# Kernel tuning notes

Hardware: AMD Instinct MI355X
Metric: run time of the kernel (lower is better)

The kernel has to match this reference:

```python
import jax, jax.numpy as jnp
import numpy as np

B, T, C = 2, 4096, 2048
HS = 64
H = C // HS            # 32 heads
D_W, D_A, D_MV, D_G = 128, 128, 64, 224
EPS_GN = 0.00064
EPS_NORM = 1e-12


def setup_inputs() -> dict:
    key = jax.random.key(0)
    ks = jax.random.split(key, 24)
    n = lambda k, s, sc=1.0: (jax.random.normal(k, s, dtype=jnp.float32) * sc)
    inp = {
        "x": n(ks[0], (B, T, C)),
        "v_first": n(ks[1], (B, T, C)),
        "y": n(ks[2], (B, T, C)),
        # token-shift mixing coefficients [1,1,C]
        "x_r": n(ks[3], (1, 1, C), 0.1), "x_w": n(ks[4], (1, 1, C), 0.1),
        "x_k": n(ks[5], (1, 1, C), 0.1), "x_v": n(ks[6], (1, 1, C), 0.1),
        "x_a": n(ks[7], (1, 1, C), 0.1), "x_g": n(ks[8], (1, 1, C), 0.1),
        # decay LoRA
        "w0": n(ks[9], (1, 1, C), 0.5) - 3.0,
        "w1": n(ks[10], (C, D_W), 0.02), "w2": n(ks[11], (D_W, C), 0.02),
        # in-context-rate LoRA
        "a0": n(ks[12], (1, 1, C), 0.2),
        "a1": n(ks[13], (C, D_A), 0.02), "a2": n(ks[14], (D_A, C), 0.02),
        # value-mix LoRA
        "v0": n(ks[15], (1, 1, C), 0.2) + 0.73,
        "v1": n(ks[16], (C, D_MV), 0.02), "v2": n(ks[17], (D_MV, C), 0.02),
        # gate LoRA
        "g1": n(ks[18], (C, D_G), 0.02), "g2": n(ks[19], (D_G, C), 0.02),
        "k_k": jnp.full((1, 1, C), 0.71, dtype=jnp.float32),
        "k_a": jnp.full((1, 1, C), 1.02, dtype=jnp.float32),
        "r_k": jnp.full((H, HS), -0.04, dtype=jnp.float32),
        # square projections
        "W_r": n(ks[20], (C, C), 0.5 / C ** 0.5),
        "W_k": n(ks[21], (C, C), 0.05 / C ** 0.5),
        "W_v": n(ks[22], (C, C), 0.5 / C ** 0.5),
        "W_o": n(ks[23], (C, C), 0.02),
        "ln_g": jnp.ones((C,), dtype=jnp.float32),
        "ln_b": jnp.zeros((C,), dtype=jnp.float32),
    }
    return inp


def reference(x, v_first, y, x_r, x_w, x_k, x_v, x_a, x_g,
              w0, w1, w2, a0, a1, a2, v0, v1, v2, g1, g2,
              k_k, k_a, r_k, W_r, W_k, W_v, W_o, ln_g, ln_b):
    Bx, Tx, Cx = x.shape
    Hn, hs = r_k.shape

    # ---- project ----
    xx = jnp.pad(x[:, :-1, :], ((0, 0), (1, 0), (0, 0))) - x  # time_shift_1(x) - x
    xr = x + xx * x_r
    xw = x + xx * x_w
    xk = x + xx * x_k
    xv = x + xx * x_v
    xa = x + xx * x_a
    xg = x + xx * x_g

    r = xr @ W_r.T
    w = -jax.nn.softplus(-(w0 + jnp.tanh(xw @ w1) @ w2)) - 0.5
    k = xk @ W_k.T
    v = xv @ W_v.T
    # layer_id == 1 (> 0): mix with v_first
    v = v + (v_first - v) * jax.nn.sigmoid(v0 + (xv @ v1) @ v2)
    a = jax.nn.sigmoid(a0 + (xa @ a1) @ a2)
    g = jax.nn.sigmoid(xg @ g1) @ g2

    kk = k * k_k
    kkh = kk.reshape(Bx, Tx, Hn, hs)
    nrm = jnp.sqrt(jnp.sum(kkh * kkh, axis=-1, keepdims=True))
    kk = (kkh / jnp.maximum(nrm, EPS_NORM)).reshape(Bx, Tx, Cx)
    k = k * (1.0 + (a - 1.0) * k_a)

    # ---- post_kernel ----
    yh = y.reshape(Bx, Tx, Hn, hs)
    mu = jnp.mean(yh, axis=-1, keepdims=True)
    var = jnp.mean((yh - mu) ** 2, axis=-1, keepdims=True)
    yn = ((yh - mu) / jnp.sqrt(var + EPS_GN)).reshape(Bx, Tx, Cx)
    yn = yn * ln_g + ln_b

    rh = r.reshape(Bx, Tx, Hn, hs)
    kh = k.reshape(Bx, Tx, Hn, hs)
    vh = v.reshape(Bx, Tx, Hn, hs)
    dot = jnp.sum(rh * kh * r_k, axis=-1, keepdims=True)  # [B,T,H,1]
    y2 = yn + (dot * vh).reshape(Bx, Tx, Cx)
    out = (y2 * g) @ W_o.T
    return out, w, a, kk
```

## Files before the change

### kernel.cpp

```cpp
#include <hip/hip_runtime.h>
#include <math.h>

typedef unsigned short u16;
typedef __attribute__((ext_vector_type(8))) short short8;
typedef __attribute__((ext_vector_type(4))) float floatx4;
typedef __attribute__((ext_vector_type(4))) unsigned short ushort4v;
typedef __attribute__((ext_vector_type(8))) unsigned short ushort8v;

#define DEV static __device__ __forceinline__

DEV u16 f2b(float f) {
  unsigned u = __builtin_bit_cast(unsigned, f);
  u += 0x7fffu + ((u >> 16) & 1u);
  return (u16)(u >> 16);
}
DEV float b2f(u16 h) { return __builtin_bit_cast(float, ((unsigned)h) << 16); }

DEV void gld16(const u16* g, u16* l) {
  __builtin_amdgcn_global_load_lds((__attribute__((address_space(1))) void*)(g),
                                   (__attribute__((address_space(3))) void*)(l), 16, 0, 0);
}

__global__ __launch_bounds__(256) void ew_mix(
    const float* __restrict__ x,
    const float* __restrict__ cr, const float* __restrict__ ck,
    const float* __restrict__ cv, const float* __restrict__ cw,
    const float* __restrict__ ca, const float* __restrict__ cg,
    u16* __restrict__ oxr, u16* __restrict__ oxk, u16* __restrict__ oxv,
    u16* __restrict__ oxw, u16* __restrict__ oxa, u16* __restrict__ oxg)
{
  const long idx = (long)blockIdx.x * 256 + threadIdx.x;
  const long row = idx >> 8;
  const int c8 = (int)(idx & 255) << 3;
  const long off = (row << 11) + c8;
  const floatx4 xa_ = *(const floatx4*)(x + off);
  const floatx4 xb_ = *(const floatx4*)(x + off + 4);
  floatx4 pa = (floatx4)0.f, pb = (floatx4)0.f;
  if ((row & 4095) != 0) {
    pa = *(const floatx4*)(x + off - 2048);
    pb = *(const floatx4*)(x + off - 2044);
  }
  floatx4 da, db;
#pragma unroll
  for (int i = 0; i < 4; ++i) { da[i] = pa[i] - xa_[i]; db[i] = pb[i] - xb_[i]; }
#define EMIT(cp, op) {                                                         \
    const floatx4 c0 = *(const floatx4*)(cp + c8);                             \
    const floatx4 c1 = *(const floatx4*)(cp + c8 + 4);                         \
    ushort8v o;                                                                \
    _Pragma("unroll")                                                          \
    for (int i = 0; i < 4; ++i) {                                              \
      o[i]     = f2b(xa_[i] + da[i] * c0[i]);                                  \
      o[4 + i] = f2b(xb_[i] + db[i] * c1[i]);                                  \
    }                                                                          \
    *(ushort8v*)(op + off) = o; }
  EMIT(cr, oxr); EMIT(ck, oxk); EMIT(cv, oxv);
  EMIT(cw, oxw); EMIT(ca, oxa); EMIT(cg, oxg);
#undef EMIT
}

__global__ __launch_bounds__(256) void transpose_cast(
    const float* __restrict__ w1, const float* __restrict__ a1,
    const float* __restrict__ v1, const float* __restrict__ g1,
    const float* __restrict__ w2, const float* __restrict__ a2,
    const float* __restrict__ v2, const float* __restrict__ g2,
    u16* __restrict__ w1T, u16* __restrict__ a1T, u16* __restrict__ v1T,
    u16* __restrict__ g1T, u16* __restrict__ w2T, u16* __restrict__ a2T,
    u16* __restrict__ v2T, u16* __restrict__ g2T,
    const float* __restrict__ Wr, const float* __restrict__ Wk,
    const float* __restrict__ Wv, const float* __restrict__ Wo,
    u16* __restrict__ Wr16, u16* __restrict__ Wk16,
    u16* __restrict__ Wv16, u16* __restrict__ Wo16)
{
  const long idx = (long)blockIdx.x * 256 + threadIdx.x;
  if (blockIdx.y >= 8) {
    const float* s; u16* d;
    switch (blockIdx.y) {
      case 8:  s = Wr; d = Wr16; break;
      case 9:  s = Wk; d = Wk16; break;
      case 10: s = Wv; d = Wv16; break;
      default: s = Wo; d = Wo16; break;
    }
    const long i = idx * 8;
    const float4 a = *(const float4*)(s + i);
    const float4 b = *(const float4*)(s + i + 4);
    ushort4v lo = { f2b(a.x), f2b(a.y), f2b(a.z), f2b(a.w) };
    ushort4v hi = { f2b(b.x), f2b(b.y), f2b(b.z), f2b(b.w) };
    *(ushort4v*)(d + i) = lo;
    *(ushort4v*)(d + i + 4) = hi;
    return;
  }
  const float* src; u16* dst; int sk, sn, dn, dk;
  switch (blockIdx.y) {
    case 0: src = w1; dst = w1T; sk = 2048; sn = 128; dn = 128;  dk = 2048; break;
    case 1: src = a1; dst = a1T; sk = 2048; sn = 128; dn = 128;  dk = 2048; break;
    case 2: src = v1; dst = v1T; sk = 2048; sn = 64;  dn = 128;  dk = 2048; break;
    case 3: src = g1; dst = g1T; sk = 2048; sn = 224; dn = 256;  dk = 2048; break;
    case 4: src = w2; dst = w2T; sk = 128;  sn = 2048; dn = 2048; dk = 128; break;
    case 5: src = a2; dst = a2T; sk = 128;  sn = 2048; dn = 2048; dk = 128; break;
    case 6: src = v2; dst = v2T; sk = 64;   sn = 2048; dn = 2048; dk = 128; break;
    default:src = g2; dst = g2T; sk = 224;  sn = 2048; dn = 2048; dk = 256; break;
  }
  const long total = (long)dn * dk;
  if (idx >= total) return;
  const int n = (int)(idx / dk), k = (int)(idx % dk);
  float v = 0.f;
  if (k < sk && n < sn) v = src[(long)k * sn + n];
  dst[idx] = f2b(v);
}

#define GEMM128_BODY(Abase, Bbase, K)                                          \
  floatx4 acc[4][4];                                                           \
  _Pragma("unroll")                                                            \
  for (int i = 0; i < 4; ++i)                                                  \
    _Pragma("unroll")                                                          \
    for (int jq = 0; jq < 4; ++jq) acc[i][jq] = (floatx4)0.f;                  \
  const int nK = (K) >> 6;                                                     \
  for (int kt = 0; kt < nK; ++kt) {                                            \
    const int k0 = kt << 6;                                                    \
    __syncthreads();                                                           \
    _Pragma("unroll")                                                          \
    for (int i = 0; i < 4; ++i) {                                              \
      const int c = i * 256 + tid;                                             \
      const int row = c >> 3;                                                  \
      const int sch = (c & 7) ^ (row & 7);                                     \
      const long goff = (long)row * (K) + k0 + sch * 8;                        \
      const int lbase = (i * 256 + wave * 64) * 8;                             \
      gld16((Abase) + goff, &sA[lbase]);                                       \
      gld16((Bbase) + goff, &sB[lbase]);                                       \
    }                                                                          \
    asm volatile("s_waitcnt vmcnt(0)" ::: "memory");                           \
    __syncthreads();                                                           \
    _Pragma("unroll")                                                          \
    for (int ks = 0; ks < 2; ++ks) {                                           \
      short8 af[4], bfr[4];                                                    \
      _Pragma("unroll")                                                        \
      for (int mi = 0; mi < 4; ++mi) {                                         \
        const int row = wm * 64 + mi * 16 + lrow;                              \
        const int ch = (ks * 4 + lkg) ^ (row & 7);                             \
        af[mi] = *(const short8*)&sA[row * 64 + ch * 8];                       \
      }                                                                        \
      _Pragma("unroll")                                                        \
      for (int ni = 0; ni < 4; ++ni) {                                         \
        const int row = wn * 64 + ni * 16 + lrow;                              \
        const int ch = (ks * 4 + lkg) ^ (row & 7);                             \
        bfr[ni] = *(const short8*)&sB[row * 64 + ch * 8];                      \
      }                                                                        \
      _Pragma("unroll")                                                        \
      for (int mi = 0; mi < 4; ++mi)                                           \
        _Pragma("unroll")                                                      \
        for (int ni = 0; ni < 4; ++ni)                                         \
          acc[mi][ni] = __builtin_amdgcn_mfma_f32_16x16x32_bf16(af[mi], bfr[ni], acc[mi][ni], 0, 0, 0); \
    }                                                                          \
  }

__global__ __launch_bounds__(256, 2) void gemm_s1(
    const u16* __restrict__ xw, const u16* __restrict__ w1T, u16* __restrict__ hw,
    const u16* __restrict__ xa, const u16* __restrict__ a1T, u16* __restrict__ ha,
    const u16* __restrict__ xv, const u16* __restrict__ v1T, u16* __restrict__ hv,
    const u16* __restrict__ xg, const u16* __restrict__ g1T, u16* __restrict__ hg)
{
  __shared__ __align__(16) u16 sA[128 * 64];
  __shared__ __align__(16) u16 sB[128 * 64];
  const int bid = blockIdx.x;
  const int jid = (bid < 64) ? 0 : (bid < 128) ? 1 : (bid < 192) ? 2 : 3;
  const u16* A = (jid == 0) ? xw : (jid == 1) ? xa : (jid == 2) ? xv : xg;
  const u16* B = (jid == 0) ? w1T : (jid == 1) ? a1T : (jid == 2) ? v1T : g1T;
  u16* Cv = (jid == 0) ? hw : (jid == 1) ? ha : (jid == 2) ? hv : hg;
  const int N = (jid == 3) ? 256 : 128;
  const int lb = bid - ((jid == 0) ? 0 : (jid == 1) ? 64 : (jid == 2) ? 128 : 192);
  const int tid = threadIdx.x;
  const int wave = tid >> 6, lane = tid & 63;
  const int lrow = lane & 15, lkg = lane >> 4;
  const int wm = wave >> 1, wn = wave & 1;
  const int nbn = N >> 7;
  const int bm = lb / nbn, bn = lb % nbn;
  const u16* Abase = A + (long)bm * 128 * 2048;
  const u16* Bbase = B + (long)bn * 128 * 2048;

  GEMM128_BODY(Abase, Bbase, 2048)

  const int row0 = bm * 128 + wm * 64 + lkg * 4;
  const int col0 = bn * 128 + wn * 64 + lrow;
#pragma unroll
  for (int mi = 0; mi < 4; ++mi)
#pragma unroll
    for (int ni = 0; ni < 4; ++ni) {
      const int col = col0 + ni * 16;
#pragma unroll
      for (int r = 0; r < 4; ++r) {
        const long o = (long)(row0 + mi * 16 + r) * N + col;
        float v = acc[mi][ni][r];
        if (jid == 0) v = tanhf(v);
        else if (jid == 3) v = 1.f / (1.f + expf(-v));
        Cv[o] = f2b(v);
      }
    }
}

__global__ __launch_bounds__(256, 2) void gemm_s2(
    const u16* __restrict__ hw, const u16* __restrict__ w2T, float* __restrict__ wsec, const float* __restrict__ w0,
    const u16* __restrict__ ha, const u16* __restrict__ a2T, float* __restrict__ asec, const float* __restrict__ a0,
    const u16* __restrict__ hv, const u16* __restrict__ v2T, u16* __restrict__ vs, const float* __restrict__ v0,
    const u16* __restrict__ hg, const u16* __restrict__ g2T, u16* __restrict__ gb)
{
  __shared__ __align__(16) u16 sA[128 * 64];
  __shared__ __align__(16) u16 sB[128 * 64];
  const int jid = blockIdx.x >> 10;
  const int lb = blockIdx.x & 1023;
  const u16* A = (jid == 0) ? hw : (jid == 1) ? ha : (jid == 2) ? hv : hg;
  const u16* B = (jid == 0) ? w2T : (jid == 1) ? a2T : (jid == 2) ? v2T : g2T;
  const float* bias = (jid == 0) ? w0 : (jid == 1) ? a0 : v0;
  const int K = (jid == 3) ? 256 : 128;
  const int tid = threadIdx.x;
  const int wave = tid >> 6, lane = tid & 63;
  const int lrow = lane & 15, lkg = lane >> 4;
  const int wm = wave >> 1, wn = wave & 1;
  const int bm = lb >> 4, bn = lb & 15;
  const u16* Abase = A + (long)bm * 128 * K;
  const u16* Bbase = B + (long)bn * 128 * K;

  GEMM128_BODY(Abase, Bbase, K)

  const int row0 = bm * 128 + wm * 64 + lkg * 4;
  const int col0 = bn * 128 + wn * 64 + lrow;
#pragma unroll
  for (int mi = 0; mi < 4; ++mi)
#pragma unroll
    for (int ni = 0; ni < 4; ++ni) {
      const int col = col0 + ni * 16;
#pragma unroll
      for (int r = 0; r < 4; ++r) {
        const long o = (long)(row0 + mi * 16 + r) * 2048 + col;
        const float v = acc[mi][ni][r];
        if (jid == 0) {
          const float zz = -(v + bias[col]);
          const float sp = fmaxf(zz, 0.f) + log1pf(expf(-fabsf(zz)));
          wsec[o] = -sp - 0.5f;
        } else if (jid == 1) {
          asec[o] = 1.f / (1.f + expf(-(v + bias[col])));
        } else if (jid == 2) {
          vs[o] = f2b(1.f / (1.f + expf(-(v + bias[col]))));
        } else {
          gb[o] = f2b(v);
        }
      }
    }
}

template<int OP>
__global__ __launch_bounds__(512, 2) void gemm256(
    const u16* __restrict__ A0, const u16* __restrict__ B0, void* __restrict__ C0,
    const u16* __restrict__ A1, const u16* __restrict__ B1, void* __restrict__ C1,
    const u16* __restrict__ A2, const u16* __restrict__ B2, void* __restrict__ C2)
{
  __shared__ __align__(16) u16 lds[8 * 8192];
  const int tid = threadIdx.x;
  const int wave = tid >> 6, lane = tid & 63;
  const int lrow = lane & 15, lq = lane >> 4;
  const int wm = wave >> 2, wn = wave & 3;
  const int job = blockIdx.x >> 8;
  const int d = blockIdx.x & 255;
  const int lb = ((d & 7) << 5) | (d >> 3);
  const int bm = lb >> 3, bn = lb & 7;

  const u16* Aj = (job == 0) ? A0 : ((job == 1) ? A1 : A2);
  const u16* Bj = (job == 0) ? B0 : ((job == 1) ? B1 : B2);
  void* Cj      = (job == 0) ? C0 : ((job == 1) ? C1 : C2);

  const u16* __restrict__ Ab = Aj + (long)bm * 256 * 2048;
  const u16* __restrict__ Bb = Bj + (long)bn * 256 * 2048;

  int srco[2], dsto[2];
#pragma unroll
  for (int l = 0; l < 2; ++l) {
    const int c = l * 512 + tid;
    const int row = c >> 2, q = c & 3;
    const int qs = q ^ ((row >> 1) & 3);
    srco[l] = row * 2048 + qs * 8;
    dsto[l] = (l * 512 + wave * 64) * 8;
  }
  int offA[2][4], offB[4];
#pragma unroll
  for (int qm = 0; qm < 2; ++qm)
#pragma unroll
    for (int mi = 0; mi < 4; ++mi) {
      const int r = wm * 128 + qm * 64 + mi * 16 + lrow;
      offA[qm][mi] = r * 32 + (lq ^ ((r >> 1) & 3)) * 8;
    }
#pragma unroll
  for (int ni = 0; ni < 4; ++ni) {
    const int r = wn * 64 + ni * 16 + lrow;
    offB[ni] = r * 32 + (lq ^ ((r >> 1) & 3)) * 8;
  }

  floatx4 acc[8][4];
#pragma unroll
  for (int i = 0; i < 8; ++i)
#pragma unroll
    for (int jq = 0; jq < 4; ++jq) acc[i][jq] = (floatx4)0.f;

#define STAGE(sU, slot) {                                                  \
    const int t_ = (sU) >> 2, j_ = (sU) & 3;                               \
    const u16* base_ = (j_ & 1) ? Bb : Ab;                                 \
    const int kofs_ = t_ * 64 + ((j_ & 2) ? 32 : 0);                       \
    gld16(base_ + srco[0] + kofs_, &lds[(slot) * 8192 + dsto[0]]);         \
    gld16(base_ + srco[1] + kofs_, &lds[(slot) * 8192 + dsto[1]]);         \
  }

#pragma unroll
  for (int s = 0; s < 6; ++s) STAGE(s, s);
  asm volatile("s_waitcnt vmcnt(4)" ::: "memory");
  asm volatile("s_barrier" ::: "memory");

#define SEC(P, sA_, sB_, sS0, sS1)                                             \
  {                                                                            \
    short8 af0[4], af1[4], bfv[4];                                             \
    _Pragma("unroll")                                                          \
    for (int mi = 0; mi < 4; ++mi)                                             \
      af0[mi] = *(const short8*)&lds[(sA_) * 8192 + offA[0][mi]];              \
    _Pragma("unroll")                                                          \
    for (int ni = 0; ni < 4; ++ni)                                             \
      bfv[ni] = *(const short8*)&lds[(sB_) * 8192 + offB[ni]];                 \
    _Pragma("unroll")                                                          \
    for (int mi = 0; mi < 4; ++mi)                                             \
      af1[mi] = *(const short8*)&lds[(sA_) * 8192 + offA[1][mi]];              \
    if ((P) < 61) { asm volatile("s_waitcnt vmcnt(4)" ::: "memory"); }         \
    else          { asm volatile("s_waitcnt vmcnt(0)" ::: "memory"); }         \
    asm volatile("s_barrier" ::: "memory");                                    \
    if ((P) <= 60) {                                                           \
      STAGE(2 * (P) + 6, sS0);                                                 \
      STAGE(2 * (P) + 7, sS1);                                                 \
    }                                                                          \
    _Pragma("unroll")                                                          \
    for (int mi = 0; mi < 4; ++mi)                                             \
      _Pragma("unroll")                                                        \
      for (int ni = 0; ni < 4; ++ni)                                           \
        acc[mi][ni] = __builtin_amdgcn_mfma_f32_16x16x32_bf16(af0[mi], bfv[ni], acc[mi][ni], 0, 0, 0); \
    _Pragma("unroll")                                                          \
    for (int mi = 0; mi < 4; ++mi)                                             \
      _Pragma("unroll")                                                        \
      for (int ni = 0; ni < 4; ++ni)                                           \
        acc[4 + mi][ni] = __builtin_amdgcn_mfma_f32_16x16x32_bf16(af1[mi], bfv[ni], acc[4 + mi][ni], 0, 0, 0); \
  }

  for (int pp = 0; pp < 64; pp += 4) {
    SEC(pp,     0, 1, 6, 7);
    SEC(pp + 1, 2, 3, 0, 1);
    SEC(pp + 2, 4, 5, 2, 3);
    SEC(pp + 3, 6, 7, 4, 5);
  }
#undef SEC
#undef STAGE

  const long row0 = (long)bm * 256 + wm * 128 + lq * 4;
  const int col0 = bn * 256 + wn * 64 + lrow;
#pragma unroll
  for (int mi = 0; mi < 8; ++mi) {
#pragma unroll
    for (int ni = 0; ni < 4; ++ni) {
      const int col = col0 + ni * 16;
#pragma unroll
      for (int r = 0; r < 4; ++r) {
        const long o = (row0 + mi * 16 + r) * 2048 + col;
        const float v = acc[mi][ni][r];
        if constexpr (OP == 0) ((float*)Cj)[o] = v;
        else ((u16*)Cj)[o] = f2b(v);
      }
    }
  }
}

DEV float wsum16(float v) {
  v += __shfl_xor(v, 1);  v += __shfl_xor(v, 2);
  v += __shfl_xor(v, 4);  v += __shfl_xor(v, 8);
  return v;
}

__global__ __launch_bounds__(256) void ew_head(
    const u16* __restrict__ r16, const u16* __restrict__ k16,
    float* __restrict__ kkout,
    const float* __restrict__ abuf,
    const u16* __restrict__ v0buf, const u16* __restrict__ vsbuf,
    const u16* __restrict__ gbuf,
    const float* __restrict__ y, const float* __restrict__ vfirst,
    const float* __restrict__ kkc, const float* __restrict__ kac,
    const float* __restrict__ rk, const float* __restrict__ lng,
    const float* __restrict__ lnb, u16* __restrict__ z)
{
  const int tid = threadIdx.x;
  const long gh = (long)blockIdx.x * 16 + (tid >> 4);
  const long m = gh >> 5;
  const int h = (int)(gh & 31);
  const int li = tid & 15;
  const int c = h * 64 + li * 4;
  const long off = (m << 11) + c;

  const ushort4v k0p = *(const ushort4v*)(k16 + off);
  const floatx4 av   = *(const floatx4*)(abuf + off);
  const floatx4 kkcv = *(const floatx4*)(kkc + c);
  const floatx4 kacv = *(const floatx4*)(kac + c);
  float k0[4], kf[4], kr[4];
  float ss = 0.f;
#pragma unroll
  for (int i = 0; i < 4; ++i) {
    k0[i] = b2f(k0p[i]);
    kf[i] = k0[i] * (1.f + (av[i] - 1.f) * kacv[i]);
    kr[i] = k0[i] * kkcv[i];
    ss += kr[i] * kr[i];
  }
  const float nrm = sqrtf(wsum16(ss));
  const float rn = 1.f / fmaxf(nrm, 1e-12f);
  floatx4 kkv;
#pragma unroll
  for (int i = 0; i < 4; ++i) kkv[i] = kr[i] * rn;
  *(floatx4*)(kkout + off) = kkv;

  const floatx4 yv = *(const floatx4*)(y + off);
  const float mu = wsum16(yv[0] + yv[1] + yv[2] + yv[3]) * 0.015625f;
  float dy[4], sv2 = 0.f;
#pragma unroll
  for (int i = 0; i < 4; ++i) { dy[i] = yv[i] - mu; sv2 += dy[i] * dy[i]; }
  const float var = wsum16(sv2) * 0.015625f;
  const float rs = rsqrtf(var + 0.00064f);
  const floatx4 lngv = *(const floatx4*)(lng + c);
  const floatx4 lnbv = *(const floatx4*)(lnb + c);
  float yn[4];
#pragma unroll
  for (int i = 0; i < 4; ++i) yn[i] = dy[i] * rs * lngv[i] + lnbv[i];

  const ushort4v rp = *(const ushort4v*)(r16 + off);
  const floatx4 rkv = *(const floatx4*)(rk + c);
  float dd = 0.f;
#pragma unroll
  for (int i = 0; i < 4; ++i) dd += b2f(rp[i]) * kf[i] * rkv[i];
  const float dot = wsum16(dd);

  const ushort4v v0p = *(const ushort4v*)(v0buf + off);
  const ushort4v vsp = *(const ushort4v*)(vsbuf + off);
  const floatx4 vfv  = *(const floatx4*)(vfirst + off);
  const ushort4v gp  = *(const ushort4v*)(gbuf + off);
  ushort4v zo;
#pragma unroll
  for (int i = 0; i < 4; ++i) {
    const float v0v = b2f(v0p[i]);
    const float vv = v0v + (vfv[i] - v0v) * b2f(vsp[i]);
    zo[i] = f2b((yn[i] + dot * vv) * b2f(gp[i]));
  }
  *(ushort4v*)(z + off) = zo;
}

extern "C" void kernel_launch(void* const* d_in, const int* in_sizes, int n_in,
                              void* d_out, int out_size, void* d_ws, size_t ws_size,
                              hipStream_t stream)
{
  (void)in_sizes; (void)out_size;
  if (n_in < 29) return;
  const int Mrows = 8192;
  const long C = 2048;
  const long MB_ = (long)Mrows * C;

  const float* x   = (const float*)d_in[0];
  const float* vf  = (const float*)d_in[1];
  const float* y   = (const float*)d_in[2];
  const float* x_r = (const float*)d_in[3];
  const float* x_w = (const float*)d_in[4];
  const float* x_k = (const float*)d_in[5];
  const float* x_v = (const float*)d_in[6];
  const float* x_a = (const float*)d_in[7];
  const float* x_g = (const float*)d_in[8];
  const float* w0  = (const float*)d_in[9];
  const float* w1  = (const float*)d_in[10];
  const float* w2  = (const float*)d_in[11];
  const float* a0  = (const float*)d_in[12];
  const float* a1  = (const float*)d_in[13];
  const float* a2  = (const float*)d_in[14];
  const float* v0  = (const float*)d_in[15];
  const float* v1  = (const float*)d_in[16];
  const float* v2  = (const float*)d_in[17];
  const float* g1  = (const float*)d_in[18];
  const float* g2  = (const float*)d_in[19];
  const float* k_k = (const float*)d_in[20];
  const float* k_a = (const float*)d_in[21];
  const float* r_k = (const float*)d_in[22];
  const float* W_r = (const float*)d_in[23];
  const float* W_k = (const float*)d_in[24];
  const float* W_v = (const float*)d_in[25];
  const float* W_o = (const float*)d_in[26];
  const float* lng = (const float*)d_in[27];
  const float* lnb = (const float*)d_in[28];

  float* out_sec = (float*)d_out;
  float* w_sec   = out_sec + MB_;
  float* a_sec   = w_sec + MB_;
  float* kk_sec  = a_sec + MB_;

  u16* k16 = (u16*)out_sec;
  u16* r16 = (u16*)out_sec + MB_;
  u16* Wr16 = (u16*)w_sec;
  u16* Wk16 = Wr16 + C * C;
  u16* Wv16 = Wk16 + C * C;

  u16* p = (u16*)d_ws;
  u16* xr = p;            p += MB_;
  u16* xk = p;            p += MB_;
  u16* xv = p;            p += MB_;
  u16* xw = p;            p += MB_;
  u16* xa = p;            p += MB_;
  u16* xg = p;            p += MB_;
  u16* Wo16 = p;          p += C * C;
  u16* w1T = p;           p += 128 * C;
  u16* a1T = p;           p += 128 * C;
  u16* v1T = p;           p += 128 * C;
  u16* g1T = p;           p += 256 * C;
  u16* w2T = p;           p += C * 128;
  u16* a2T = p;           p += C * 128;
  u16* v2T = p;           p += C * 128;
  u16* g2T = p;           p += C * 256;
  u16* hw  = p;           p += (long)Mrows * 128;
  u16* ha  = p;           p += (long)Mrows * 128;
  u16* hv  = p;           p += (long)Mrows * 128;
  u16* hg  = p;           p += (long)Mrows * 256;
  const size_t need = (size_t)((char*)p - (char*)d_ws);
  if (ws_size < need) return;

  u16* v0buf = xg;
  u16* zbuf  = xk;
  u16* vsbuf = xw;
  u16* gbuf  = xa;

  ew_mix<<<8192, 256, 0, stream>>>(x, x_r, x_k, x_v, x_w, x_a, x_g,
                                   xr, xk, xv, xw, xa, xg);
  transpose_cast<<<dim3(2048, 12), 256, 0, stream>>>(
      w1, a1, v1, g1, w2, a2, v2, g2,
      w1T, a1T, v1T, g1T, w2T, a2T, v2T, g2T,
      W_r, W_k, W_v, W_o, Wr16, Wk16, Wv16, Wo16);
  gemm_s1<<<320, 256, 0, stream>>>(xw, w1T, hw, xa, a1T, ha,
                                   xv, v1T, hv, xg, g1T, hg);
  gemm256<1><<<768, 512, 0, stream>>>(xr, Wr16, r16,
                                      xk, Wk16, k16,
                                      xv, Wv16, v0buf);
  gemm_s2<<<4096, 256, 0, stream>>>(hw, w2T, w_sec, w0,
                                    ha, a2T, a_sec, a0,
                                    hv, v2T, vsbuf, v0,
                                    hg, g2T, gbuf);
  ew_head<<<16384, 256, 0, stream>>>(r16, k16, kk_sec, a_sec, v0buf, vsbuf, gbuf,
                                     y, vf, k_k, k_a, r_k, lng, lnb, zbuf);
  gemm256<0><<<256, 512, 0, stream>>>(zbuf, Wo16, out_sec,
                                      zbuf, Wo16, out_sec,
                                      zbuf, Wo16, out_sec);
}
```

Measured before the change: 670.5 us.

## Use 4-wave 256x256 GEMM blocks with 128x128 warp tiles and register double-buffered fragments

The 256x256 bf16 GEMM moves from 8 waves (128x64 per wave) to 4 waves (128x128 per wave), which raises MFMA work per LDS fragment load. It also double-buffers the A and B fragments in registers, so fragments for the next K-step are read from LDS while the current MFMAs issue. Each thread now issues 4 global-to-LDS loads per stage, and the wait counts are adjusted to match. The cost is a much larger register footprint (64 accumulators plus 32 fragment registers) and occupancy of one 256-thread block per CU, which risks spills or leaving little latency hiding.

```diff
diff --git a/kernel.cpp b/kernel.cpp
--- a/kernel.cpp
+++ b/kernel.cpp
@@ -248,7 +248,7 @@
 }
 
 template<int OP>
-__global__ __launch_bounds__(512, 2) void gemm256(
+__global__ __launch_bounds__(256, 1) void gemm256(
     const u16* __restrict__ A0, const u16* __restrict__ B0, void* __restrict__ C0,
     const u16* __restrict__ A1, const u16* __restrict__ B1, void* __restrict__ C1,
     const u16* __restrict__ A2, const u16* __restrict__ B2, void* __restrict__ C2)
@@ -257,7 +257,7 @@
   const int tid = threadIdx.x;
   const int wave = tid >> 6, lane = tid & 63;
   const int lrow = lane & 15, lq = lane >> 4;
-  const int wm = wave >> 2, wn = wave & 3;
+  const int wm = wave >> 1, wn = wave & 1;
   const int job = blockIdx.x >> 8;
   const int d = blockIdx.x & 255;
   const int lb = ((d & 7) << 5) | (d >> 3);
@@ -270,62 +270,55 @@
   const u16* __restrict__ Ab = Aj + (long)bm * 256 * 2048;
   const u16* __restrict__ Bb = Bj + (long)bn * 256 * 2048;
 
-  int srco[2], dsto[2];
-#pragma unroll
-  for (int l = 0; l < 2; ++l) {
-    const int c = l * 512 + tid;
+  int srco[4], dsto[4];
+#pragma unroll
+  for (int l = 0; l < 4; ++l) {
+    const int c = l * 256 + tid;
     const int row = c >> 2, q = c & 3;
     const int qs = q ^ ((row >> 1) & 3);
     srco[l] = row * 2048 + qs * 8;
-    dsto[l] = (l * 512 + wave * 64) * 8;
-  }
-  int offA[2][4], offB[4];
-#pragma unroll
-  for (int qm = 0; qm < 2; ++qm)
-#pragma unroll
-    for (int mi = 0; mi < 4; ++mi) {
-      const int r = wm * 128 + qm * 64 + mi * 16 + lrow;
-      offA[qm][mi] = r * 32 + (lq ^ ((r >> 1) & 3)) * 8;
-    }
-#pragma unroll
-  for (int ni = 0; ni < 4; ++ni) {
-    const int r = wn * 64 + ni * 16 + lrow;
+    dsto[l] = (l * 256 + wave * 64) * 8;
+  }
+  int offA[8], offB[8];
+#pragma unroll
+  for (int mi = 0; mi < 8; ++mi) {
+    const int r = wm * 128 + mi * 16 + lrow;
+    offA[mi] = r * 32 + (lq ^ ((r >> 1) & 3)) * 8;
+  }
+#pragma unroll
+  for (int ni = 0; ni < 8; ++ni) {
+    const int r = wn * 128 + ni * 16 + lrow;
     offB[ni] = r * 32 + (lq ^ ((r >> 1) & 3)) * 8;
   }
 
-  floatx4 acc[8][4];
+  floatx4 acc[8][8];
 #pragma unroll
   for (int i = 0; i < 8; ++i)
 #pragma unroll
-    for (int jq = 0; jq < 4; ++jq) acc[i][jq] = (floatx4)0.f;
+    for (int jq = 0; jq < 8; ++jq) acc[i][jq] = (floatx4)0.f;
 
 #define STAGE(sU, slot) {                                                  \
     const int t_ = (sU) >> 2, j_ = (sU) & 3;                               \
     const u16* base_ = (j_ & 1) ? Bb : Ab;                                 \
     const int kofs_ = t_ * 64 + ((j_ & 2) ? 32 : 0);                       \
-    gld16(base_ + srco[0] + kofs_, &lds[(slot) * 8192 + dsto[0]]);         \
-    gld16(base_ + srco[1] + kofs_, &lds[(slot) * 8192 + dsto[1]]);         \
+    _Pragma("unroll")                                                      \
+    for (int l_ = 0; l_ < 4; ++l_)                                         \
+      gld16(base_ + srco[l_] + kofs_, &lds[(slot) * 8192 + dsto[l_]]);     \
   }
 
 #pragma unroll
   for (int s = 0; s < 6; ++s) STAGE(s, s);
-  asm volatile("s_waitcnt vmcnt(4)" ::: "memory");
+  asm volatile("s_waitcnt vmcnt(8)" ::: "memory");
   asm volatile("s_barrier" ::: "memory");
 
-#define SEC(P, sA_, sB_, sS0, sS1)                                             \
+  short8 fa[8], fb[8], ga[8], gb_[8];
+#pragma unroll
+  for (int mi = 0; mi < 8; ++mi) fa[mi] = *(const short8*)&lds[0 * 8192 + offA[mi]];
+#pragma unroll
+  for (int ni = 0; ni < 8; ++ni) fb[ni] = *(const short8*)&lds[1 * 8192 + offB[ni]];
+
+#define SEC(P, curA, curB, nxtA, nxtB, rdA, rdB, sS0, sS1)                     \
   {                                                                            \
-    short8 af0[4], af1[4], bfv[4];                                             \
-    _Pragma("unroll")                                                          \
-    for (int mi = 0; mi < 4; ++mi)                                             \
-      af0[mi] = *(const short8*)&lds[(sA_) * 8192 + offA[0][mi]];              \
-    _Pragma("unroll")                                                          \
-    for (int ni = 0; ni < 4; ++ni)                                             \
-      bfv[ni] = *(const short8*)&lds[(sB_) * 8192 + offB[ni]];                 \
-    _Pragma("unroll")                                                          \
-    for (int mi = 0; mi < 4; ++mi)                                             \
-      af1[mi] = *(const short8*)&lds[(sA_) * 8192 + offA[1][mi]];              \
-    if ((P) < 61) { asm volatile("s_waitcnt vmcnt(4)" ::: "memory"); }         \
-    else          { asm volatile("s_waitcnt vmcnt(0)" ::: "memory"); }         \
     asm volatile("s_barrier" ::: "memory");                                    \
     if ((P) <= 60) {                                                           \
       STAGE(2 * (P) + 6, sS0);                                                 \
@@ -334,30 +327,40 @@
     _Pragma("unroll")                                                          \
     for (int mi = 0; mi < 4; ++mi)                                             \
       _Pragma("unroll")                                                        \
-      for (int ni = 0; ni < 4; ++ni)                                           \
-        acc[mi][ni] = __builtin_amdgcn_mfma_f32_16x16x32_bf16(af0[mi], bfv[ni], acc[mi][ni], 0, 0, 0); \
+      for (int ni = 0; ni < 8; ++ni)                                           \
+        acc[mi][ni] = __builtin_amdgcn_mfma_f32_16x16x32_bf16(curA[mi], curB[ni], acc[mi][ni], 0, 0, 0); \
+    if ((P) < 63) {                                                            \
+      _Pragma("unroll")                                                        \
+      for (int mi = 0; mi < 8; ++mi)                                           \
+        nxtA[mi] = *(const short8*)&lds[(rdA) * 8192 + offA[mi]];              \
+      _Pragma("unroll")                                                        \
+      for (int ni = 0; ni < 8; ++ni)                                           \
+        nxtB[ni] = *(const short8*)&lds[(rdB) * 8192 + offB[ni]];              \
+    }                                                                          \
     _Pragma("unroll")                                                          \
-    for (int mi = 0; mi < 4; ++mi)                                             \
-      _Pragma("unroll")                                                        \
-      for (int ni = 0; ni < 4; ++ni)                                           \
-        acc[4 + mi][ni] = __builtin_amdgcn_mfma_f32_16x16x32_bf16(af1[mi], bfv[ni], acc[4 + mi][ni], 0, 0, 0); \
+    for (int mi = 4; mi < 8; ++mi)                                             \
+      _Pragma("unroll")                                                        \
+      for (int ni = 0; ni < 8; ++ni)                                           \
+        acc[mi][ni] = __builtin_amdgcn_mfma_f32_16x16x32_bf16(curA[mi], curB[ni], acc[mi][ni], 0, 0, 0); \
+    if ((P) < 62) { asm volatile("s_waitcnt vmcnt(8)" ::: "memory"); }         \
+    else          { asm volatile("s_waitcnt vmcnt(0)" ::: "memory"); }         \
   }
 
   for (int pp = 0; pp < 64; pp += 4) {
-    SEC(pp,     0, 1, 6, 7);
-    SEC(pp + 1, 2, 3, 0, 1);
-    SEC(pp + 2, 4, 5, 2, 3);
-    SEC(pp + 3, 6, 7, 4, 5);
+    SEC(pp,     fa, fb, ga, gb_, 2, 3, 6, 7);
+    SEC(pp + 1, ga, gb_, fa, fb, 4, 5, 0, 1);
+    SEC(pp + 2, fa, fb, ga, gb_, 6, 7, 2, 3);
+    SEC(pp + 3, ga, gb_, fa, fb, 0, 1, 4, 5);
   }
 #undef SEC
 #undef STAGE
 
   const long row0 = (long)bm * 256 + wm * 128 + lq * 4;
-  const int col0 = bn * 256 + wn * 64 + lrow;
+  const int col0 = bn * 256 + wn * 128 + lrow;
 #pragma unroll
   for (int mi = 0; mi < 8; ++mi) {
 #pragma unroll
-    for (int ni = 0; ni < 4; ++ni) {
+    for (int ni = 0; ni < 8; ++ni) {
       const int col = col0 + ni * 16;
 #pragma unroll
       for (int r = 0; r < 4; ++r) {
@@ -536,7 +539,7 @@
       W_r, W_k, W_v, W_o, Wr16, Wk16, Wv16, Wo16);
   gemm_s1<<<320, 256, 0, stream>>>(xw, w1T, hw, xa, a1T, ha,
                                    xv, v1T, hv, xg, g1T, hg);
-  gemm256<1><<<768, 512, 0, stream>>>(xr, Wr16, r16,
+  gemm256<1><<<768, 256, 0, stream>>>(xr, Wr16, r16,
                                       xk, Wk16, k16,
                                       xv, Wv16, v0buf);
   gemm_s2<<<4096, 256, 0, stream>>>(hw, w2T, w_sec, w0,
@@ -545,7 +548,7 @@
                                     hg, g2T, gbuf);
   ew_head<<<16384, 256, 0, stream>>>(r16, k16, kk_sec, a_sec, v0buf, vsbuf, gbuf,
                                      y, vf, k_k, k_a, r_k, lng, lnb, zbuf);
-  gemm256<0><<<256, 512, 0, stream>>>(zbuf, Wo16, out_sec,
+  gemm256<0><<<256, 256, 0, stream>>>(zbuf, Wo16, out_sec,
                                       zbuf, Wo16, out_sec,
                                       zbuf, Wo16, out_sec);
 }
```

New measurement: 798.8 us. 19.1% more time.
